# Performance work log

Measured on AMD Instinct MI355X. Metric: run time of the kernel, lower is better.

Reference implementation:

```python
import jax, jax.numpy as jnp
import numpy as np

B, N, F = 64, 1024, 1
C = 50          # GCNConv channels
H = 512         # fc1 units
K = 10          # classes


def setup_inputs() -> dict:
    key = jax.random.key(0)
    ks = jax.random.split(key, 6)
    x = jax.random.normal(ks[0], (B, N, F), dtype=jnp.float32)
    # GCN-normalized adjacency stand-in: nonnegative dense [B,N,N]
    a = jax.random.uniform(ks[1], (B, N, N), dtype=jnp.float32)
    w1 = jax.random.normal(ks[2], (F, C), dtype=jnp.float32) * (1.0 / np.sqrt(F))
    b1 = jnp.zeros((C,), jnp.float32)
    w2 = jax.random.normal(ks[3], (C, C), dtype=jnp.float32) * (1.0 / np.sqrt(C))
    b2 = jnp.zeros((C,), jnp.float32)
    wf1 = jax.random.normal(ks[4], (C, H), dtype=jnp.float32) * (1.0 / np.sqrt(C))
    bf1 = jnp.zeros((H,), jnp.float32)
    wf2 = jax.random.normal(ks[5], (H, K), dtype=jnp.float32) * (1.0 / np.sqrt(H))
    bf2 = jnp.zeros((K,), jnp.float32)
    return {"x": x, "a": a, "w1": w1, "b1": b1, "w2": w2, "b2": b2,
            "wf1": wf1, "bf1": bf1, "wf2": wf2, "bf2": bf2}


def gcn_conv(x, a, w, b):
    # Spektral GCNConv (batch mode): activation(A @ X @ W + b)
    xw = jnp.einsum('bnf,fc->bnc', x, w)          # transform first (F small)
    return jax.nn.elu(jnp.einsum('bnm,bmc->bnc', a, xw) + b)


def reference(x, a, w1, b1, w2, b2, wf1, bf1, wf2, bf2):
    h = gcn_conv(x, a, w1, b1)                    # [B,N,C]
    h = gcn_conv(h, a, w2, b2)                    # [B,N,C]
    pooled = jnp.sum(h, axis=1)                   # GlobalSumPool -> [B,C]
    h = jax.nn.relu(pooled @ wf1 + bf1)           # [B,H]
    return jax.nn.softmax(h @ wf2 + bf2, axis=-1) # [B,K]
```

## Files before the change

kernel.cpp:

```cpp
#include <hip/hip_runtime.h>
#include <math.h>

#define BB 64
#define NN 1024
#define CC 50
#define HH 512
#define KK 10
#define DP 64

typedef short bf16x8 __attribute__((ext_vector_type(8)));
typedef float f32x4  __attribute__((ext_vector_type(4)));

__device__ __forceinline__ float elu_f(float v) { return v > 0.f ? v : expm1f(v); }

__device__ __forceinline__ void split_bf16(float f, unsigned short& hi, unsigned short& lo) {
    unsigned int u = __float_as_uint(f);
    hi = (unsigned short)(u >> 16);
    float hif = __uint_as_float(u & 0xFFFF0000u);
    lo = (unsigned short)(__float_as_uint(f - hif) >> 16);
}

__global__ __launch_bounds__(256) void k1_s_g(
        const float* __restrict__ x, const float* __restrict__ a,
        const float* __restrict__ w1, const float* __restrict__ b1,
        const float* __restrict__ w2,
        unsigned short* __restrict__ gt_hi, unsigned short* __restrict__ gt_lo)
{
    __shared__ float xs[NN];
    __shared__ float w1s[CC], b1s[CC];
    __shared__ float w2s[CC * CC];

    int tid = threadIdx.x;
    int b = blockIdx.x >> 5;
    int seg = blockIdx.x & 31;

    float4* xs4 = (float4*)xs;
    xs4[tid] = ((const float4*)(x + (size_t)b * NN))[tid];
    if (tid < CC) { w1s[tid] = w1[tid]; b1s[tid] = b1[tid]; }
    for (int i = tid; i < CC * CC; i += 256) w2s[i] = w2[i];
    __syncthreads();

    int wid = tid >> 6, lane = tid & 63;

    for (int it = 0; it < 8; ++it) {
        int n = seg * 32 + it * 4 + wid;
        const float4* arow = (const float4*)(a + ((size_t)b * NN + n) * NN);

        float acc = 0.f;
        #pragma unroll
        for (int k4 = 0; k4 < 4; ++k4) {
            float4 av = arow[k4 * 64 + lane];
            float4 xv = xs4[k4 * 64 + lane];
            acc += av.x * xv.x + av.y * xv.y + av.z * xv.z + av.w * xv.w;
        }
        #pragma unroll
        for (int off = 32; off; off >>= 1) acc += __shfl_xor(acc, off);

        float h1 = 0.f;
        if (lane < CC) h1 = elu_f(acc * w1s[lane] + b1s[lane]);

        float gacc = 0.f;
        #pragma unroll 10
        for (int c = 0; c < CC; ++c) {
            float hv = __shfl(h1, c);
            if (lane < CC) gacc += hv * w2s[c * CC + lane];
        }
        if (lane < CC) {
            unsigned short hi, lo;
            split_bf16(gacc, hi, lo);
            size_t off = ((size_t)b * DP + lane) * NN + n;
            gt_hi[off] = hi;
            gt_lo[off] = lo;
        }
    }
}

__global__ __launch_bounds__(256) void k2_mfma_pool(
        const float* __restrict__ a,
        const unsigned short* __restrict__ gt_hi,
        const unsigned short* __restrict__ gt_lo,
        const float* __restrict__ b2, float* __restrict__ pooled)
{
    __shared__ float ps[DP];

    int tid = threadIdx.x;
    int wv = tid >> 6, l = tid & 63;
    int lr = l & 15, lk = l >> 4;
    int b  = (BB - 1) - (blockIdx.x >> 3);
    int n0 = (blockIdx.x & 7) * 128 + wv * 32;

    const float* Ab = a + ((size_t)b * NN + n0) * NN;
    const unsigned short* Gh = gt_hi + (size_t)b * DP * NN;
    const unsigned short* Gl = gt_lo + (size_t)b * DP * NN;

    if (tid < DP) ps[tid] = 0.f;

    float bias[4];
    #pragma unroll
    for (int ds = 0; ds < 4; ++ds) {
        int d = ds * 16 + lr;
        bias[ds] = (d < CC) ? b2[d] : 0.f;
    }

    f32x4 acc[2][4] = {};

    for (int m0 = 0; m0 < NN; m0 += 32) {
        bf16x8 ah[2], al[2];
        #pragma unroll
        for (int s = 0; s < 2; ++s) {
            const float* ap = Ab + (size_t)(s * 16 + lr) * NN + m0 + lk * 8;
            float4 v0 = *(const float4*)(ap);
            float4 v1 = *(const float4*)(ap + 4);
            float av[8] = {v0.x, v0.y, v0.z, v0.w, v1.x, v1.y, v1.z, v1.w};
            #pragma unroll
            for (int j = 0; j < 8; ++j) {
                unsigned short hi, lo;
                split_bf16(av[j], hi, lo);
                ah[s][j] = (short)hi;
                al[s][j] = (short)lo;
            }
        }
        bf16x8 bh[4], bl[4];
        #pragma unroll
        for (int ds = 0; ds < 4; ++ds) {
            size_t off = (size_t)(ds * 16 + lr) * NN + m0 + lk * 8;
            bh[ds] = *(const bf16x8*)(Gh + off);
            bl[ds] = *(const bf16x8*)(Gl + off);
        }
        #pragma unroll
        for (int s = 0; s < 2; ++s)
            #pragma unroll
            for (int ds = 0; ds < 4; ++ds) {
                acc[s][ds] = __builtin_amdgcn_mfma_f32_16x16x32_bf16(ah[s], bh[ds], acc[s][ds], 0, 0, 0);
                acc[s][ds] = __builtin_amdgcn_mfma_f32_16x16x32_bf16(ah[s], bl[ds], acc[s][ds], 0, 0, 0);
                acc[s][ds] = __builtin_amdgcn_mfma_f32_16x16x32_bf16(al[s], bh[ds], acc[s][ds], 0, 0, 0);
            }
    }

    __syncthreads();
    #pragma unroll
    for (int ds = 0; ds < 4; ++ds) {
        int d = ds * 16 + lr;
        float s = 0.f;
        if (d < CC) {
            #pragma unroll
            for (int sb = 0; sb < 2; ++sb)
                #pragma unroll
                for (int j = 0; j < 4; ++j)
                    s += elu_f(acc[sb][ds][j] + bias[ds]);
        }
        s += __shfl_xor(s, 16);
        s += __shfl_xor(s, 32);
        if (lk == 0 && d < CC) atomicAdd(&ps[d], s);
    }
    __syncthreads();
    if (tid < CC) atomicAdd(&pooled[b * CC + tid], ps[tid]);
}

__global__ __launch_bounds__(256) void k3_fc(
        const float* __restrict__ pooled,
        const float* __restrict__ wf1, const float* __restrict__ bf1,
        const float* __restrict__ wf2, const float* __restrict__ bf2,
        float* __restrict__ out)
{
    __shared__ float p[CC];
    __shared__ float h[HH];
    __shared__ float lg[KK];
    int b = blockIdx.x, tid = threadIdx.x;

    if (tid < CC) p[tid] = pooled[b * CC + tid];
    __syncthreads();

    for (int j = tid; j < HH; j += 256) {
        float acc = bf1[j];
        #pragma unroll 10
        for (int c = 0; c < CC; ++c) acc += p[c] * wf1[c * HH + j];
        h[j] = fmaxf(acc, 0.f);
    }
    __syncthreads();

    if (tid < KK) {
        float acc = bf2[tid];
        for (int j = 0; j < HH; ++j) acc += h[j] * wf2[j * KK + tid];
        lg[tid] = acc;
    }
    __syncthreads();

    if (tid == 0) {
        float mx = lg[0];
        for (int k = 1; k < KK; ++k) mx = fmaxf(mx, lg[k]);
        float e[KK], sum = 0.f;
        for (int k = 0; k < KK; ++k) { e[k] = expf(lg[k] - mx); sum += e[k]; }
        float inv = 1.f / sum;
        for (int k = 0; k < KK; ++k) out[b * KK + k] = e[k] * inv;
    }
}

extern "C" void kernel_launch(void* const* d_in, const int* in_sizes, int n_in,
                              void* d_out, int out_size, void* d_ws, size_t ws_size,
                              hipStream_t stream) {
    const float* x   = (const float*)d_in[0];
    const float* a   = (const float*)d_in[1];
    const float* w1  = (const float*)d_in[2];
    const float* b1  = (const float*)d_in[3];
    const float* w2  = (const float*)d_in[4];
    const float* b2  = (const float*)d_in[5];
    const float* wf1 = (const float*)d_in[6];
    const float* bf1 = (const float*)d_in[7];
    const float* wf2 = (const float*)d_in[8];
    const float* bf2 = (const float*)d_in[9];
    float* out = (float*)d_out;

    float*          pooled = (float*)d_ws;
    unsigned short* gt_hi  = (unsigned short*)((char*)d_ws + (64 << 10));
    unsigned short* gt_lo  = (unsigned short*)((char*)d_ws + (64 << 10) + ((size_t)BB * DP * NN * 2));

    hipMemsetAsync(pooled, 0, BB * CC * sizeof(float), stream);
    k1_s_g<<<BB * 32, 256, 0, stream>>>(x, a, w1, b1, w2, gt_hi, gt_lo);
    k2_mfma_pool<<<BB * 8, 256, 0, stream>>>(a, gt_hi, gt_lo, b2, pooled);
    k3_fc<<<BB, 256, 0, stream>>>(pooled, wf1, bf1, wf2, bf2, out);
}
```

Baseline: 544.6 us.

## Restructure GCN stage-1 into batched phases and double k2 grid size

Stage 1 now handles 64 rows per block in separate phases: row dot products, an ELU expansion into shared memory, then a register-blocked 50x50 transform. The transposed bf16 hi/lo output is written with vectorized 16-byte stores instead of scattered 2-byte stores. Stage 2 halves rows per wave (16 instead of 32) and doubles the block count for more parallelism, at the cost of reading the G operand twice as often. The memset launch is folded into stage 1 by zeroing pooled in the seg-0 blocks.

```diff
diff --git a/kernel.cpp b/kernel.cpp
--- a/kernel.cpp
+++ b/kernel.cpp
@@ -7,6 +7,7 @@
 #define HH 512
 #define KK 10
 #define DP 64
+#define H1S 52
 
 typedef short bf16x8 __attribute__((ext_vector_type(8)));
 typedef float f32x4  __attribute__((ext_vector_type(4)));
@@ -24,54 +25,96 @@
         const float* __restrict__ x, const float* __restrict__ a,
         const float* __restrict__ w1, const float* __restrict__ b1,
         const float* __restrict__ w2,
-        unsigned short* __restrict__ gt_hi, unsigned short* __restrict__ gt_lo)
+        unsigned short* __restrict__ gt_hi, unsigned short* __restrict__ gt_lo,
+        float* __restrict__ pooled)
 {
-    __shared__ float xs[NN];
     __shared__ float w1s[CC], b1s[CC];
     __shared__ float w2s[CC * CC];
+    __shared__ float ss[64];
+    __shared__ float h1s[64 * H1S];
 
     int tid = threadIdx.x;
-    int b = blockIdx.x >> 5;
-    int seg = blockIdx.x & 31;
-
-    float4* xs4 = (float4*)xs;
-    xs4[tid] = ((const float4*)(x + (size_t)b * NN))[tid];
+    int b = blockIdx.x >> 4;
+    int seg = blockIdx.x & 15;
+    int n0 = seg * 64;
+    int wid = tid >> 6, lane = tid & 63;
+
+    if (seg == 0 && tid < CC) pooled[b * CC + tid] = 0.f;
     if (tid < CC) { w1s[tid] = w1[tid]; b1s[tid] = b1[tid]; }
     for (int i = tid; i < CC * CC; i += 256) w2s[i] = w2[i];
-    __syncthreads();
-
-    int wid = tid >> 6, lane = tid & 63;
-
-    for (int it = 0; it < 8; ++it) {
-        int n = seg * 32 + it * 4 + wid;
-        const float4* arow = (const float4*)(a + ((size_t)b * NN + n) * NN);
-
+
+    float4 xv[4];
+    {
+        const float4* xb4 = (const float4*)(x + (size_t)b * NN);
+        #pragma unroll
+        for (int k4 = 0; k4 < 4; ++k4) xv[k4] = xb4[k4 * 64 + lane];
+    }
+    __syncthreads();
+
+    for (int it = 0; it < 16; ++it) {
+        int nl = it * 4 + wid;
+        const float4* arow = (const float4*)(a + ((size_t)b * NN + n0 + nl) * NN);
         float acc = 0.f;
         #pragma unroll
         for (int k4 = 0; k4 < 4; ++k4) {
             float4 av = arow[k4 * 64 + lane];
-            float4 xv = xs4[k4 * 64 + lane];
-            acc += av.x * xv.x + av.y * xv.y + av.z * xv.z + av.w * xv.w;
+            acc += av.x * xv[k4].x + av.y * xv[k4].y + av.z * xv[k4].z + av.w * xv[k4].w;
         }
         #pragma unroll
         for (int off = 32; off; off >>= 1) acc += __shfl_xor(acc, off);
-
-        float h1 = 0.f;
-        if (lane < CC) h1 = elu_f(acc * w1s[lane] + b1s[lane]);
-
-        float gacc = 0.f;
-        #pragma unroll 10
-        for (int c = 0; c < CC; ++c) {
-            float hv = __shfl(h1, c);
-            if (lane < CC) gacc += hv * w2s[c * CC + lane];
-        }
-        if (lane < CC) {
+        if (lane == 0) ss[nl] = acc;
+    }
+    __syncthreads();
+
+    {
+        int c = tid & 63, nb = tid >> 6;
+        if (c < CC) {
+            float w1c = w1s[c], b1c = b1s[c];
+            #pragma unroll
+            for (int it = 0; it < 16; ++it) {
+                int nl = it * 4 + nb;
+                h1s[nl * H1S + c] = elu_f(ss[nl] * w1c + b1c);
+            }
+        }
+    }
+    __syncthreads();
+
+    {
+        int d = tid & 63, nb = tid >> 6;
+        float accg[16] = {};
+        if (d < CC) {
+            const float* h1base = &h1s[(size_t)nb * 16 * H1S];
+            for (int cq = 0; cq < 48; cq += 4) {
+                float w2q0 = w2s[(cq + 0) * CC + d];
+                float w2q1 = w2s[(cq + 1) * CC + d];
+                float w2q2 = w2s[(cq + 2) * CC + d];
+                float w2q3 = w2s[(cq + 3) * CC + d];
+                #pragma unroll
+                for (int it = 0; it < 16; ++it) {
+                    float4 h4 = *(const float4*)(h1base + it * H1S + cq);
+                    accg[it] += h4.x * w2q0 + h4.y * w2q1 + h4.z * w2q2 + h4.w * w2q3;
+                }
+            }
+            #pragma unroll
+            for (int c = 48; c < CC; ++c) {
+                float w2v = w2s[c * CC + d];
+                #pragma unroll
+                for (int it = 0; it < 16; ++it)
+                    accg[it] += h1base[it * H1S + c] * w2v;
+            }
+        }
+        bf16x8 h0, h1v, l0, l1;
+        #pragma unroll
+        for (int j = 0; j < 8; ++j) {
             unsigned short hi, lo;
-            split_bf16(gacc, hi, lo);
-            size_t off = ((size_t)b * DP + lane) * NN + n;
-            gt_hi[off] = hi;
-            gt_lo[off] = lo;
-        }
+            split_bf16(accg[j], hi, lo);      h0[j] = (short)hi; l0[j] = (short)lo;
+            split_bf16(accg[8 + j], hi, lo);  h1v[j] = (short)hi; l1[j] = (short)lo;
+        }
+        size_t off = ((size_t)b * DP + d) * NN + n0 + nb * 16;
+        *(bf16x8*)(gt_hi + off)     = h0;
+        *(bf16x8*)(gt_hi + off + 8) = h1v;
+        *(bf16x8*)(gt_lo + off)     = l0;
+        *(bf16x8*)(gt_lo + off + 8) = l1;
     }
 }
 
@@ -86,14 +129,15 @@
     int tid = threadIdx.x;
     int wv = tid >> 6, l = tid & 63;
     int lr = l & 15, lk = l >> 4;
-    int b  = (BB - 1) - (blockIdx.x >> 3);
-    int n0 = (blockIdx.x & 7) * 128 + wv * 32;
+    int b  = (BB - 1) - (blockIdx.x >> 4);
+    int n0 = (blockIdx.x & 15) * 64 + wv * 16;
 
     const float* Ab = a + ((size_t)b * NN + n0) * NN;
     const unsigned short* Gh = gt_hi + (size_t)b * DP * NN;
     const unsigned short* Gl = gt_lo + (size_t)b * DP * NN;
 
     if (tid < DP) ps[tid] = 0.f;
+    __syncthreads();
 
     float bias[4];
     #pragma unroll
@@ -102,13 +146,13 @@
         bias[ds] = (d < CC) ? b2[d] : 0.f;
     }
 
-    f32x4 acc[2][4] = {};
-
+    f32x4 acc[4] = {};
+
+    #pragma unroll 2
     for (int m0 = 0; m0 < NN; m0 += 32) {
-        bf16x8 ah[2], al[2];
-        #pragma unroll
-        for (int s = 0; s < 2; ++s) {
-            const float* ap = Ab + (size_t)(s * 16 + lr) * NN + m0 + lk * 8;
+        bf16x8 ah, al;
+        {
+            const float* ap = Ab + (size_t)lr * NN + m0 + lk * 8;
             float4 v0 = *(const float4*)(ap);
             float4 v1 = *(const float4*)(ap + 4);
             float av[8] = {v0.x, v0.y, v0.z, v0.w, v1.x, v1.y, v1.z, v1.w};
@@ -116,8 +160,8 @@
             for (int j = 0; j < 8; ++j) {
                 unsigned short hi, lo;
                 split_bf16(av[j], hi, lo);
-                ah[s][j] = (short)hi;
-                al[s][j] = (short)lo;
+                ah[j] = (short)hi;
+                al[j] = (short)lo;
             }
         }
         bf16x8 bh[4], bl[4];
@@ -128,26 +172,21 @@
             bl[ds] = *(const bf16x8*)(Gl + off);
         }
         #pragma unroll
-        for (int s = 0; s < 2; ++s)
-            #pragma unroll
-            for (int ds = 0; ds < 4; ++ds) {
-                acc[s][ds] = __builtin_amdgcn_mfma_f32_16x16x32_bf16(ah[s], bh[ds], acc[s][ds], 0, 0, 0);
-                acc[s][ds] = __builtin_amdgcn_mfma_f32_16x16x32_bf16(ah[s], bl[ds], acc[s][ds], 0, 0, 0);
-                acc[s][ds] = __builtin_amdgcn_mfma_f32_16x16x32_bf16(al[s], bh[ds], acc[s][ds], 0, 0, 0);
-            }
-    }
-
-    __syncthreads();
+        for (int ds = 0; ds < 4; ++ds) {
+            acc[ds] = __builtin_amdgcn_mfma_f32_16x16x32_bf16(ah, bh[ds], acc[ds], 0, 0, 0);
+            acc[ds] = __builtin_amdgcn_mfma_f32_16x16x32_bf16(ah, bl[ds], acc[ds], 0, 0, 0);
+            acc[ds] = __builtin_amdgcn_mfma_f32_16x16x32_bf16(al, bh[ds], acc[ds], 0, 0, 0);
+        }
+    }
+
     #pragma unroll
     for (int ds = 0; ds < 4; ++ds) {
         int d = ds * 16 + lr;
         float s = 0.f;
         if (d < CC) {
             #pragma unroll
-            for (int sb = 0; sb < 2; ++sb)
-                #pragma unroll
-                for (int j = 0; j < 4; ++j)
-                    s += elu_f(acc[sb][ds][j] + bias[ds]);
+            for (int j = 0; j < 4; ++j)
+                s += elu_f(acc[ds][j] + bias[ds]);
         }
         s += __shfl_xor(s, 16);
         s += __shfl_xor(s, 32);
@@ -215,8 +254,7 @@
     unsigned short* gt_hi  = (unsigned short*)((char*)d_ws + (64 << 10));
     unsigned short* gt_lo  = (unsigned short*)((char*)d_ws + (64 << 10) + ((size_t)BB * DP * NN * 2));
 
-    hipMemsetAsync(pooled, 0, BB * CC * sizeof(float), stream);
-    k1_s_g<<<BB * 32, 256, 0, stream>>>(x, a, w1, b1, w2, gt_hi, gt_lo);
-    k2_mfma_pool<<<BB * 8, 256, 0, stream>>>(a, gt_hi, gt_lo, b2, pooled);
+    k1_s_g<<<BB * 16, 256, 0, stream>>>(x, a, w1, b1, w2, gt_hi, gt_lo, pooled);
+    k2_mfma_pool<<<BB * 16, 256, 0, stream>>>(a, gt_hi, gt_lo, b2, pooled);
     k3_fc<<<BB, 256, 0, stream>>>(pooled, wf1, bf1, wf2, bf2, out);
 }
```

Measured after the change: 570.9 us. 1.05x slower.
